# Kernel optimization log

Measured on AMD Instinct MI355X. Metric: run time of the kernel, lower is better.

## Reference

```python
import math
import jax, jax.numpy as jnp
import numpy as np

B, T, HID = 8, 2048, 1536
H, D = 8, 192
CHUNK, PAST, FUT = 12, 12, 0
CTX = CHUNK + PAST + FUT          # 24
F = PAST + FUT + 1                # 13 relative positions
CAP = 50.0
INVALID = -1.0e9


def setup_inputs() -> dict:
    key = jax.random.key(0)
    k1, k2, k3 = jax.random.split(key, 3)
    x = jax.random.normal(k1, (B, T, HID), dtype=jnp.float32)
    mask = jnp.zeros((B, T), dtype=bool)  # True = invalid/padding
    # causal validity: key offset (c - PAST) relative to query w must lie in [-PAST, FUT]
    w = jnp.arange(CHUNK)[:, None]
    c = jnp.arange(CTX)[None, :]
    causal_valid_mask = (c >= w) & (c <= w + PAST + FUT)  # [CHUNK, CTX]
    W_qkv = jax.random.normal(k2, (HID, 3 * HID), dtype=jnp.float32) * 0.02
    W_pos = jax.random.normal(k3, (HID, HID), dtype=jnp.float32) * 0.02
    per_dim_scale = jnp.zeros((D,), dtype=jnp.float32)
    return {"x": x, "mask": mask, "causal_valid_mask": causal_valid_mask,
            "W_qkv": W_qkv, "W_pos": W_pos, "per_dim_scale": per_dim_scale}


def _extract_block_context(z, U):
    # pad time dim left=PAST, right=FUT+CHUNK-1, then frame with step CHUNK, len CTX
    pad = ((0, 0), (PAST, FUT + CHUNK - 1)) + ((0, 0),) * (z.ndim - 2)
    zp = jnp.pad(z, pad)
    idx = jnp.arange(U)[:, None] * CHUNK + jnp.arange(CTX)[None, :]  # [U, CTX]
    return zp[:, idx]  # [B, U, CTX, ...]


def reference(x, mask, causal_valid_mask, W_qkv, W_pos, per_dim_scale):
    b, t, _ = x.shape
    qkv = x @ W_qkv
    q, k, v = jnp.split(qkv, 3, axis=-1)
    q = q.reshape(b, t, H, D)
    k = k.reshape(b, t, H, D)
    v = v.reshape(b, t, H, D)

    q_scale = D ** (-0.5) / math.log(2.0)
    k_scale = math.log(1.0 + math.e) / math.log(2.0)
    q = q * q_scale * jax.nn.softplus(per_dim_scale)  # per-dim scale on queries
    k = k * k_scale

    U = -(-t // CHUNK)  # ceil
    pad_q = U * CHUNK - t
    qb = jnp.pad(q, ((0, 0), (0, pad_q), (0, 0), (0, 0))).reshape(b, U, CHUNK, H, D)
    kb = _extract_block_context(k, U)            # [B,U,CTX,H,D]
    vb = _extract_block_context(v, U)            # [B,U,CTX,H,D]
    valid = _extract_block_context(~mask, U)     # [B,U,CTX]

    # ---- relative position embedding (Transformer-XL style) ----
    pos = jnp.arange(PAST, -FUT - 1, -1, dtype=jnp.float32)  # [F]
    nts = HID // 2
    inv_ts = jnp.exp(jnp.arange(nts, dtype=jnp.float32) * (-(math.log(10000.0) / (nts - 1))))
    st = pos[:, None] * inv_ts[None, :]
    emb = jnp.concatenate([jnp.sin(st), jnp.cos(st)], axis=-1)  # [F, HID]
    sin_emb = (emb @ W_pos).reshape(F, H, D)

    term_ac = jnp.einsum('buwhd,buchd->bhuwc', qb, kb)     # content-content
    term_bd = jnp.einsum('buwhd,fhd->bhuwf', qb, sin_emb)  # content-position
    # relative shift: pad last dim to CTX+1, flatten, slice, reshape
    pad_amt = CTX + 1 - F
    tb = jnp.pad(term_bd, ((0, 0),) * 4 + ((0, pad_amt),))
    tb = tb.reshape(b, H, U, CHUNK * (CTX + 1))[..., :CHUNK * CTX]
    tb = tb.reshape(b, H, U, CHUNK, CTX)

    logits = term_ac + tb
    logits = jnp.tanh(logits / CAP) * CAP  # softcap
    cond = valid[:, None, :, None, :] & causal_valid_mask[None, None, None, :, :]
    logits = jnp.where(cond, logits, INVALID)
    probs = jax.nn.softmax(logits, axis=-1)
    out = jnp.einsum('bhuwc,buchd->buwhd', probs, vb)
    return out.reshape(b, U * CHUNK, H, D)[:, :t]
```

## Files before the change

kernel.cpp:

```cpp
#include <hip/hip_runtime.h>

typedef unsigned int u32;
typedef unsigned short u16;

typedef __attribute__((ext_vector_type(8))) short bf16x8;
typedef __attribute__((ext_vector_type(4))) float f32x4;

__device__ __forceinline__ u16 f2bf(float f) {
  u32 u = __builtin_bit_cast(u32, f);
  u32 r = (u + 0x7fffu + ((u >> 16) & 1u)) >> 16;
  return (u16)r;
}
__device__ __forceinline__ float bfl(u32 u) { return __builtin_bit_cast(float, u << 16); }
__device__ __forceinline__ float bfh(u32 u) { return __builtin_bit_cast(float, u & 0xffff0000u); }

__device__ __forceinline__ void gload_lds16(const u16* g, u16* l) {
  __builtin_amdgcn_global_load_lds(
      (const __attribute__((address_space(1))) void*)g,
      (__attribute__((address_space(3))) void*)l, 16, 0, 0);
}

__global__ __launch_bounds__(256) void transp_wt(const float* __restrict__ W,
                                                 u16* __restrict__ Wt) {
  __shared__ float tile[64][68];
  int bk = blockIdx.x % 24, bn = blockIdx.x / 24;
  int k0 = bk * 64, n0 = bn * 64;
  int tid = threadIdx.x;
#pragma unroll
  for (int p = 0; p < 4; p++) {
    int idx = p * 256 + tid;
    int r = idx >> 4, c4 = idx & 15;
    *(float4*)&tile[r][c4 * 4] = *(const float4*)&W[(size_t)(k0 + r) * 4608 + n0 + c4 * 4];
  }
  __syncthreads();
#pragma unroll
  for (int p = 0; p < 2; p++) {
    int idx = p * 256 + tid;
    int rn = idx >> 3, kc = idx & 7;
    u16 pk[8];
#pragma unroll
    for (int e = 0; e < 8; e++) pk[e] = f2bf(tile[kc * 8 + e][rn]);
    *(uint4*)&Wt[(size_t)(n0 + rn) * 1536 + k0 + kc * 8] = *(const uint4*)pk;
  }
}

__global__ __launch_bounds__(256) void conv_x(const float* __restrict__ X,
                                              u16* __restrict__ Xb) {
  int i = blockIdx.x * 256 + threadIdx.x;
  const float4* xp = (const float4*)X;
  float4 a = xp[i * 2], b = xp[i * 2 + 1];
  uint4 o;
  o.x = (u32)f2bf(a.x) | ((u32)f2bf(a.y) << 16);
  o.y = (u32)f2bf(a.z) | ((u32)f2bf(a.w) << 16);
  o.z = (u32)f2bf(b.x) | ((u32)f2bf(b.y) << 16);
  o.w = (u32)f2bf(b.z) | ((u32)f2bf(b.w) << 16);
  ((uint4*)Xb)[i] = o;
}

__global__ __launch_bounds__(256) void pos_emb_part(const float* __restrict__ Wp,
                                                    float* __restrict__ part) {
  __shared__ float er[13 * 32];
  int ks = blockIdx.x % 48, nb = blockIdx.x / 48;
  int tid = threadIdx.x;
  int n = nb * 256 + tid;
  const float cfreq = 9.210340371976184f / 767.0f;
  for (int i = tid; i < 13 * 32; i += 256) {
    int f = i >> 5, kk = i & 31;
    int k = ks * 32 + kk;
    int ii = (k < 768) ? k : (k - 768);
    float fr = expf(-cfreq * (float)ii);
    float st = (float)(12 - f) * fr;
    er[f * 32 + kk] = (k < 768) ? sinf(st) : cosf(st);
  }
  __syncthreads();
  float acc[13];
#pragma unroll
  for (int f = 0; f < 13; f++) acc[f] = 0.f;
  const float* wp = Wp + (size_t)(ks * 32) * 1536 + n;
  for (int kk = 0; kk < 32; kk++) {
    float w = wp[(size_t)kk * 1536];
#pragma unroll
    for (int f = 0; f < 13; f++) acc[f] = fmaf(er[f * 32 + kk], w, acc[f]);
  }
#pragma unroll
  for (int f = 0; f < 13; f++)
    part[((size_t)ks * 13 + f) * 1536 + n] = acc[f];
}

__global__ __launch_bounds__(256) void pos_emb_red(const float* __restrict__ part,
                                                   u16* __restrict__ sembbf) {
  int idxg = blockIdx.x * 256 + threadIdx.x;
  int f = idxg / 1536, n = idxg % 1536;
  float s = 0.f;
  if (f < 13)
    for (int ks = 0; ks < 48; ks++)
      s += part[((size_t)ks * 13 + f) * 1536 + n];
  sembbf[idxg] = f2bf(s);
}

__global__ __launch_bounds__(256, 2) void gemm_qkv(const u16* __restrict__ Xb,
                                                   const u16* __restrict__ Bt,
                                                   u16* __restrict__ C,
                                                   const float* __restrict__ pds) {
  extern __shared__ u16 smem[];

  const int tid = threadIdx.x;
  const int lane = tid & 63;
  const int wv = tid >> 6;
  const int wr = wv >> 1;
  const int wc = wv & 1;
  const int lr = lane & 15;
  const int lkq = lane >> 4;
  const int sx = lr & 7;

  int bid = blockIdx.x;
  int xcd = bid & 7, idx = bid >> 3;
  int bm = xcd * 8 + idx / 36;
  int bn = idx % 36;
  int m0 = bm * 256, n0 = bn * 128;

  auto stageA = [&](int T) {
#pragma unroll
    for (int q = 0; q < 8; q++) {
      int ch = q * 256 + tid;
      int r = ch >> 3, cr = ch & 7;
      int crs = cr ^ (r & 7);
      gload_lds16(Xb + (size_t)(m0 + r) * 1536 + T * 64 + crs * 8, smem + ch * 8);
    }
  };
  auto stageB = [&](int T) {
#pragma unroll
    for (int q = 0; q < 4; q++) {
      int ch = q * 256 + tid;
      int r = ch >> 3, cr = ch & 7;
      int crs = cr ^ (r & 7);
      gload_lds16(Bt + (size_t)(n0 + r) * 1536 + T * 64 + crs * 8,
                  smem + 16384 + (T & 1) * 8192 + ch * 8);
    }
  };

  f32x4 acc[8][4];
#pragma unroll
  for (int i = 0; i < 8; i++)
#pragma unroll
    for (int j = 0; j < 4; j++) acc[i][j] = (f32x4){0.f, 0.f, 0.f, 0.f};

  stageA(0); stageB(0);
  asm volatile("s_waitcnt vmcnt(0)" ::: "memory");
  __builtin_amdgcn_s_barrier();

  for (int t = 0; t < 24; t++) {
    const int bb = 16384 + (t & 1) * 8192;

    bf16x8 af[16], bfr[4];
#pragma unroll
    for (int i = 0; i < 8; i++) {
      int R = wr * 128 + i * 16 + lr;
      af[i * 2 + 0] = *(const bf16x8*)&smem[R * 64 + (lkq ^ sx) * 8];
      af[i * 2 + 1] = *(const bf16x8*)&smem[R * 64 + ((4 + lkq) ^ sx) * 8];
    }
    asm volatile("s_waitcnt lgkmcnt(0)" ::: "memory");
    __builtin_amdgcn_s_barrier();
    if (t < 23) { stageA(t + 1); stageB(t + 1); }

#pragma unroll
    for (int j = 0; j < 4; j++) {
      int R = wc * 64 + j * 16 + lr;
      bfr[j] = *(const bf16x8*)&smem[bb + R * 64 + (lkq ^ sx) * 8];
    }
    __builtin_amdgcn_s_setprio(1);
#pragma unroll
    for (int i = 0; i < 8; i++)
#pragma unroll
      for (int j = 0; j < 4; j++)
        acc[i][j] = __builtin_amdgcn_mfma_f32_16x16x32_bf16(af[i * 2], bfr[j], acc[i][j], 0, 0, 0);
    __builtin_amdgcn_s_setprio(0);

#pragma unroll
    for (int j = 0; j < 4; j++) {
      int R = wc * 64 + j * 16 + lr;
      bfr[j] = *(const bf16x8*)&smem[bb + R * 64 + ((4 + lkq) ^ sx) * 8];
    }
    __builtin_amdgcn_s_setprio(1);
#pragma unroll
    for (int i = 0; i < 8; i++)
#pragma unroll
      for (int j = 0; j < 4; j++)
        acc[i][j] = __builtin_amdgcn_mfma_f32_16x16x32_bf16(af[i * 2 + 1], bfr[j], acc[i][j], 0, 0, 0);
    __builtin_amdgcn_s_setprio(0);

    asm volatile("s_waitcnt vmcnt(0)" ::: "memory");
    __builtin_amdgcn_s_barrier();
  }

  const float kscale = 1.8946361f;
  float scl[4];
#pragma unroll
  for (int j = 0; j < 4; j++) {
    int gcol = n0 + wc * 64 + j * 16 + lr;
    float s;
    if (gcol < 1536) s = 0.10411754f * log1pf(expf(pds[gcol % 192]));
    else if (gcol < 3072) s = kscale;
    else s = 1.0f;
    scl[j] = s;
  }
#pragma unroll
  for (int h = 0; h < 2; h++) {
    if (wr == h) {
#pragma unroll
      for (int i = 0; i < 8; i++)
#pragma unroll
        for (int j = 0; j < 4; j++) {
          int row = i * 16 + lkq * 4;
          int col = wc * 64 + j * 16 + lr;
#pragma unroll
          for (int r = 0; r < 4; r++)
            smem[(row + r) * 136 + col] = f2bf(acc[i][j][r] * scl[j]);
        }
    }
    asm volatile("s_waitcnt lgkmcnt(0)" ::: "memory");
    __builtin_amdgcn_s_barrier();
#pragma unroll
    for (int p = 0; p < 8; p++) {
      int idx2 = p * 256 + tid;
      int row = idx2 >> 4, cq = idx2 & 15;
      *(uint4*)&C[(size_t)(m0 + h * 128 + row) * 4608 + n0 + cq * 8] =
          *(const uint4*)&smem[row * 136 + cq * 8];
    }
    __builtin_amdgcn_s_barrier();
  }
}

__global__ __launch_bounds__(512) void qsemb(const u16* __restrict__ qkv,
                                             const u16* __restrict__ sembbf,
                                             float* __restrict__ bdall) {
  int tid = threadIdx.x;
  int lane = tid & 63;
  int h = tid >> 6;
  int t0 = blockIdx.x * 16;
  int arow = lane & 15, ak = lane >> 4;

  const u16* qp = qkv + (size_t)(t0 + arow) * 4608 + h * 192 + ak * 8;
  const u16* sp = sembbf + (size_t)(lane & 15) * 1536 + h * 192 + ak * 8;

  f32x4 acc = (f32x4){0.f, 0.f, 0.f, 0.f};
#pragma unroll
  for (int kt = 0; kt < 6; kt++) {
    bf16x8 a = *(const bf16x8*)(qp + kt * 32);
    bf16x8 bb = *(const bf16x8*)(sp + kt * 32);
    acc = __builtin_amdgcn_mfma_f32_16x16x32_bf16(a, bb, acc, 0, 0, 0);
  }
  int f = lane & 15;
  int rbase = (lane >> 4) * 4;
  if (f < 13) {
#pragma unroll
    for (int r = 0; r < 4; r++)
      bdall[(size_t)(t0 + rbase + r) * 104 + h * 13 + f] = acc[r];
  }
}

__global__ __launch_bounds__(256) void attn_kernel(const u16* __restrict__ qkv,
                                                   const float* __restrict__ bdall,
                                                   const unsigned char* __restrict__ mask,
                                                   float* __restrict__ out) {
  __shared__ u16 sq[24 * 200];
  __shared__ u16 sk[36 * 200];
  __shared__ u16 sv[36 * 200];
  __shared__ float lg[24 * 14];
  __shared__ int vld[36];

  int bid = blockIdx.x;
  int h = bid & 7;
  int u2 = (bid >> 3) % 86;
  int b = bid / (86 * 8);
  int tid = threadIdx.x;
  int tbase = u2 * 24;

  if (tid < 36) {
    int t = tbase + tid - 12;
    vld[tid] = (t >= 0 && t < 2048 && mask[b * 2048 + t] == 0) ? 1 : 0;
  }

  const u16* base = qkv + (size_t)b * 2048 * 4608 + h * 192;
  for (int idx = tid; idx < 576; idx += 256) {
    int w = idx / 24, g = idx % 24;
    int t = tbase + w;
    uint4 val = {0u, 0u, 0u, 0u};
    if (t < 2048) val = *(const uint4*)(base + (size_t)t * 4608 + g * 8);
    *(uint4*)&sq[w * 200 + g * 8] = val;
  }
  for (int idx = tid; idx < 1728; idx += 256) {
    int kv = idx / 864, r = idx % 864;
    int c = r / 24, g = r % 24;
    int t = tbase + c - 12;
    uint4 val = {0u, 0u, 0u, 0u};
    if (t >= 0 && t < 2048)
      val = *(const uint4*)(base + (size_t)t * 4608 + (kv ? 3072 : 1536) + g * 8);
    if (kv) *(uint4*)&sv[c * 200 + g * 8] = val;
    else    *(uint4*)&sk[c * 200 + g * 8] = val;
  }
  __syncthreads();

  for (int idx = tid; idx < 312; idx += 256) {
    int w = idx % 24, f = idx / 24;
    int c = w + f;
    int t = tbase + w;
    float l = -1e9f;
    if (vld[c] && t < 2048) {
      float ac = 0.f;
      const u16* qp = &sq[w * 200];
      const u16* kp = &sk[c * 200];
#pragma unroll 4
      for (int i = 0; i < 24; i++) {
        uint4 qa = *(const uint4*)(qp + i * 8);
        uint4 kb = *(const uint4*)(kp + i * 8);
        ac = fmaf(bfl(qa.x), bfl(kb.x), ac);
        ac = fmaf(bfh(qa.x), bfh(kb.x), ac);
        ac = fmaf(bfl(qa.y), bfl(kb.y), ac);
        ac = fmaf(bfh(qa.y), bfh(kb.y), ac);
        ac = fmaf(bfl(qa.z), bfl(kb.z), ac);
        ac = fmaf(bfh(qa.z), bfh(kb.z), ac);
        ac = fmaf(bfl(qa.w), bfl(kb.w), ac);
        ac = fmaf(bfh(qa.w), bfh(kb.w), ac);
      }
      float bd = bdall[(size_t)(b * 2048 + t) * 104 + h * 13 + f];
      l = tanhf((ac + bd) * 0.02f) * 50.f;
    }
    lg[w * 14 + f] = l;
  }
  __syncthreads();

  if (tid < 24) {
    float m = -3e38f;
#pragma unroll
    for (int f = 0; f < 13; f++) m = fmaxf(m, lg[tid * 14 + f]);
    float s = 0.f;
#pragma unroll
    for (int f = 0; f < 13; f++) {
      float e = expf(lg[tid * 14 + f] - m);
      lg[tid * 14 + f] = e;
      s += e;
    }
    float inv = 1.f / s;
#pragma unroll
    for (int f = 0; f < 13; f++) lg[tid * 14 + f] *= inv;
  }
  __syncthreads();

  for (int idx = tid; idx < 1152; idx += 256) {
    int w = idx / 48, g = idx % 48;
    int t = tbase + w;
    if (t >= 2048) continue;
    float a0 = 0, a1 = 0, a2 = 0, a3 = 0;
#pragma unroll
    for (int f = 0; f < 13; f++) {
      float p = lg[w * 14 + f];
      uint2 vv = *(const uint2*)&sv[(w + f) * 200 + g * 4];
      a0 = fmaf(p, bfl(vv.x), a0);
      a1 = fmaf(p, bfh(vv.x), a1);
      a2 = fmaf(p, bfl(vv.y), a2);
      a3 = fmaf(p, bfh(vv.y), a3);
    }
    float4 o = {a0, a1, a2, a3};
    *(float4*)&out[(((size_t)(b * 2048 + t)) * 8 + h) * 192 + g * 4] = o;
  }
}

extern "C" void kernel_launch(void* const* d_in, const int* in_sizes, int n_in,
                              void* d_out, int out_size, void* d_ws, size_t ws_size,
                              hipStream_t stream) {
  (void)in_sizes; (void)n_in; (void)out_size; (void)ws_size;
  const float* x = (const float*)d_in[0];
  const unsigned char* mask = (const unsigned char*)d_in[1];
  const float* Wqkv = (const float*)d_in[3];
  const float* Wpos = (const float*)d_in[4];
  const float* pds = (const float*)d_in[5];
  float* out = (float*)d_out;

  char* ws = (char*)d_ws;
  u16* Wt = (u16*)ws;
  u16* qkv = (u16*)(ws + 14155776);
  u16* Xb = (u16*)(ws + 165150720);
  u16* sembbf = (u16*)(ws + 215482368);
  float* bdall = (float*)(ws + 215531520);
  float* part = (float*)(ws + 222347264);

  transp_wt<<<1728, 256, 0, stream>>>(Wqkv, Wt);
  conv_x<<<12288, 256, 0, stream>>>(x, Xb);
  pos_emb_part<<<288, 256, 0, stream>>>(Wpos, part);
  pos_emb_red<<<96, 256, 0, stream>>>(part, sembbf);
  gemm_qkv<<<2304, 256, 65536, stream>>>(Xb, Wt, qkv, pds);
  qsemb<<<1024, 512, 0, stream>>>(qkv, sembbf, bdall);
  attn_kernel<<<5504, 256, 0, stream>>>(qkv, bdall, mask, out);
}
```

Baseline: 348.6 us.

## Retile QKV GEMM to 128x288 blocks with split A/B staging

```diff
diff --git a/kernel.cpp b/kernel.cpp
--- a/kernel.cpp
+++ b/kernel.cpp
@@ -115,78 +115,85 @@
 
   int bid = blockIdx.x;
   int xcd = bid & 7, idx = bid >> 3;
-  int bm = xcd * 8 + idx / 36;
-  int bn = idx % 36;
-  int m0 = bm * 256, n0 = bn * 128;
+  int bm = xcd * 16 + idx / 16;
+  int bn = idx % 16;
+  int m0 = bm * 128, n0 = bn * 288;
 
   auto stageA = [&](int T) {
-#pragma unroll
-    for (int q = 0; q < 8; q++) {
-      int ch = q * 256 + tid;
-      int r = ch >> 3, cr = ch & 7;
-      int crs = cr ^ (r & 7);
-      gload_lds16(Xb + (size_t)(m0 + r) * 1536 + T * 64 + crs * 8, smem + ch * 8);
-    }
-  };
-  auto stageB = [&](int T) {
 #pragma unroll
     for (int q = 0; q < 4; q++) {
       int ch = q * 256 + tid;
       int r = ch >> 3, cr = ch & 7;
       int crs = cr ^ (r & 7);
+      gload_lds16(Xb + (size_t)(m0 + r) * 1536 + T * 64 + crs * 8,
+                  smem + (T & 1) * 8192 + ch * 8);
+    }
+  };
+  auto stageB = [&](int T) {
+#pragma unroll
+    for (int q = 0; q < 9; q++) {
+      int ch = q * 256 + tid;
+      int r = ch >> 3, cr = ch & 7;
+      int crs = cr ^ (r & 7);
       gload_lds16(Bt + (size_t)(n0 + r) * 1536 + T * 64 + crs * 8,
-                  smem + 16384 + (T & 1) * 8192 + ch * 8);
+                  smem + 16384 + ch * 8);
     }
   };
 
-  f32x4 acc[8][4];
-#pragma unroll
-  for (int i = 0; i < 8; i++)
-#pragma unroll
-    for (int j = 0; j < 4; j++) acc[i][j] = (f32x4){0.f, 0.f, 0.f, 0.f};
+  f32x4 acc[4][9];
+#pragma unroll
+  for (int i = 0; i < 4; i++)
+#pragma unroll
+    for (int j = 0; j < 9; j++) acc[i][j] = (f32x4){0.f, 0.f, 0.f, 0.f};
 
   stageA(0); stageB(0);
   asm volatile("s_waitcnt vmcnt(0)" ::: "memory");
   __builtin_amdgcn_s_barrier();
 
   for (int t = 0; t < 24; t++) {
-    const int bb = 16384 + (t & 1) * 8192;
-
-    bf16x8 af[16], bfr[4];
-#pragma unroll
-    for (int i = 0; i < 8; i++) {
-      int R = wr * 128 + i * 16 + lr;
-      af[i * 2 + 0] = *(const bf16x8*)&smem[R * 64 + (lkq ^ sx) * 8];
-      af[i * 2 + 1] = *(const bf16x8*)&smem[R * 64 + ((4 + lkq) ^ sx) * 8];
+    const int ab = (t & 1) * 8192;
+
+    if (t < 23) stageA(t + 1);
+
+    bf16x8 af[4], bfr[9];
+#pragma unroll
+    for (int i = 0; i < 4; i++) {
+      int R = wr * 64 + i * 16 + lr;
+      af[i] = *(const bf16x8*)&smem[ab + R * 64 + (lkq ^ sx) * 8];
+    }
+#pragma unroll
+    for (int j = 0; j < 9; j++) {
+      int R = wc * 144 + j * 16 + lr;
+      bfr[j] = *(const bf16x8*)&smem[16384 + R * 64 + (lkq ^ sx) * 8];
+    }
+    __builtin_amdgcn_s_setprio(1);
+#pragma unroll
+    for (int i = 0; i < 4; i++)
+#pragma unroll
+      for (int j = 0; j < 9; j++)
+        acc[i][j] = __builtin_amdgcn_mfma_f32_16x16x32_bf16(af[i], bfr[j], acc[i][j], 0, 0, 0);
+    __builtin_amdgcn_s_setprio(0);
+
+#pragma unroll
+    for (int i = 0; i < 4; i++) {
+      int R = wr * 64 + i * 16 + lr;
+      af[i] = *(const bf16x8*)&smem[ab + R * 64 + ((4 + lkq) ^ sx) * 8];
+    }
+#pragma unroll
+    for (int j = 0; j < 9; j++) {
+      int R = wc * 144 + j * 16 + lr;
+      bfr[j] = *(const bf16x8*)&smem[16384 + R * 64 + ((4 + lkq) ^ sx) * 8];
     }
     asm volatile("s_waitcnt lgkmcnt(0)" ::: "memory");
     __builtin_amdgcn_s_barrier();
-    if (t < 23) { stageA(t + 1); stageB(t + 1); }
-
-#pragma unroll
-    for (int j = 0; j < 4; j++) {
-      int R = wc * 64 + j * 16 + lr;
-      bfr[j] = *(const bf16x8*)&smem[bb + R * 64 + (lkq ^ sx) * 8];
-    }
+    if (t < 23) stageB(t + 1);
+
     __builtin_amdgcn_s_setprio(1);
 #pragma unroll
-    for (int i = 0; i < 8; i++)
-#pragma unroll
-      for (int j = 0; j < 4; j++)
-        acc[i][j] = __builtin_amdgcn_mfma_f32_16x16x32_bf16(af[i * 2], bfr[j], acc[i][j], 0, 0, 0);
-    __builtin_amdgcn_s_setprio(0);
-
-#pragma unroll
-    for (int j = 0; j < 4; j++) {
-      int R = wc * 64 + j * 16 + lr;
-      bfr[j] = *(const bf16x8*)&smem[bb + R * 64 + ((4 + lkq) ^ sx) * 8];
-    }
-    __builtin_amdgcn_s_setprio(1);
-#pragma unroll
-    for (int i = 0; i < 8; i++)
-#pragma unroll
-      for (int j = 0; j < 4; j++)
-        acc[i][j] = __builtin_amdgcn_mfma_f32_16x16x32_bf16(af[i * 2 + 1], bfr[j], acc[i][j], 0, 0, 0);
+    for (int i = 0; i < 4; i++)
+#pragma unroll
+      for (int j = 0; j < 9; j++)
+        acc[i][j] = __builtin_amdgcn_mfma_f32_16x16x32_bf16(af[i], bfr[j], acc[i][j], 0, 0, 0);
     __builtin_amdgcn_s_setprio(0);
 
     asm volatile("s_waitcnt vmcnt(0)" ::: "memory");
@@ -194,10 +201,10 @@
   }
 
   const float kscale = 1.8946361f;
-  float scl[4];
-#pragma unroll
-  for (int j = 0; j < 4; j++) {
-    int gcol = n0 + wc * 64 + j * 16 + lr;
+  float scl[9];
+#pragma unroll
+  for (int j = 0; j < 9; j++) {
+    int gcol = n0 + wc * 144 + j * 16 + lr;
     float s;
     if (gcol < 1536) s = 0.10411754f * log1pf(expf(pds[gcol % 192]));
     else if (gcol < 3072) s = kscale;
@@ -205,29 +212,23 @@
     scl[j] = s;
   }
 #pragma unroll
-  for (int h = 0; h < 2; h++) {
-    if (wr == h) {
-#pragma unroll
-      for (int i = 0; i < 8; i++)
-#pragma unroll
-        for (int j = 0; j < 4; j++) {
-          int row = i * 16 + lkq * 4;
-          int col = wc * 64 + j * 16 + lr;
-#pragma unroll
-          for (int r = 0; r < 4; r++)
-            smem[(row + r) * 136 + col] = f2bf(acc[i][j][r] * scl[j]);
-        }
-    }
-    asm volatile("s_waitcnt lgkmcnt(0)" ::: "memory");
-    __builtin_amdgcn_s_barrier();
-#pragma unroll
-    for (int p = 0; p < 8; p++) {
-      int idx2 = p * 256 + tid;
-      int row = idx2 >> 4, cq = idx2 & 15;
-      *(uint4*)&C[(size_t)(m0 + h * 128 + row) * 4608 + n0 + cq * 8] =
-          *(const uint4*)&smem[row * 136 + cq * 8];
-    }
-    __builtin_amdgcn_s_barrier();
+  for (int i = 0; i < 4; i++)
+#pragma unroll
+    for (int j = 0; j < 9; j++) {
+      int row = wr * 64 + i * 16 + lkq * 4;
+      int col = wc * 144 + j * 16 + lr;
+#pragma unroll
+      for (int r = 0; r < 4; r++)
+        smem[(row + r) * 296 + col] = f2bf(acc[i][j][r] * scl[j]);
+    }
+  asm volatile("s_waitcnt lgkmcnt(0)" ::: "memory");
+  __builtin_amdgcn_s_barrier();
+#pragma unroll
+  for (int p = 0; p < 18; p++) {
+    int idx2 = p * 256 + tid;
+    int row = idx2 / 36, cq = idx2 % 36;
+    *(uint4*)&C[(size_t)(m0 + row) * 4608 + n0 + cq * 8] =
+        *(const uint4*)&smem[row * 296 + cq * 8];
   }
 }
 
@@ -389,7 +390,7 @@
   conv_x<<<12288, 256, 0, stream>>>(x, Xb);
   pos_emb_part<<<288, 256, 0, stream>>>(Wpos, part);
   pos_emb_red<<<96, 256, 0, stream>>>(part, sembbf);
-  gemm_qkv<<<2304, 256, 65536, stream>>>(Xb, Wt, qkv, pds);
+  gemm_qkv<<<2048, 256, 75776, stream>>>(Xb, Wt, qkv, pds);
   qsemb<<<1024, 512, 0, stream>>>(qkv, sembbf, bdall);
   attn_kernel<<<5504, 256, 0, stream>>>(qkv, bdall, mask, out);
 }
```

New measurement: 351.7 us. About the same (+0.9%).
